# Kernel optimization log

Hardware: AMD Instinct MI355X
Metric: run time of the kernel (lower is better)

Reference implementation:

```python
import jax, jax.numpy as jnp
import numpy as np
from jax import lax

B, S, I, K = 64, 512, 50, 4
H_FC, OUT, H_R = 1024, 128, 512


def setup_inputs() -> dict:
    key = jax.random.key(0)
    ks = jax.random.split(key, 24)
    inp = {}
    inp["x"] = jax.random.normal(ks[0], (B, S, I), dtype=jnp.float32)
    # col 0 = mu, col 1 = sigma (divisor); uniform(0,1) shifted away from 0 for stability
    fp = jax.random.uniform(ks[1], (I * K, 2), dtype=jnp.float32)
    inp["fuzzy_params"] = fp.at[:, 1].add(0.5)
    # FC stack: (I*K -> H_FC), (H_FC -> H_FC) x (num_fc-2=2), (H_FC -> OUT)
    dims = [(H_FC, I * K), (H_FC, H_FC), (H_FC, H_FC), (OUT, H_FC)]
    for j, (o, i) in enumerate(dims):
        inp[f"fc{j}_w"] = jax.random.normal(ks[2 + 2 * j], (o, i), dtype=jnp.float32) * 0.02
        inp[f"fc{j}_b"] = jnp.zeros((o,), dtype=jnp.float32)
    # 2-layer Elman RNN (tanh), batch_first
    inp["w_ih0"] = jax.random.normal(ks[12], (H_R, OUT), dtype=jnp.float32) * 0.04
    inp["w_hh0"] = jax.random.normal(ks[13], (H_R, H_R), dtype=jnp.float32) * 0.04
    inp["b_ih0"] = jnp.zeros((H_R,), dtype=jnp.float32)
    inp["b_hh0"] = jnp.zeros((H_R,), dtype=jnp.float32)
    inp["w_ih1"] = jax.random.normal(ks[14], (H_R, H_R), dtype=jnp.float32) * 0.04
    inp["w_hh1"] = jax.random.normal(ks[15], (H_R, H_R), dtype=jnp.float32) * 0.04
    inp["b_ih1"] = jnp.zeros((H_R,), dtype=jnp.float32)
    inp["b_hh1"] = jnp.zeros((H_R,), dtype=jnp.float32)
    return inp


def _rnn_layer(inp, w_ih, w_hh, b_ih, b_hh):
    # inp: [B,S,D] -> [B,S,H]; precompute input projection, scan recurrence over time
    pre = jnp.einsum("bsd,hd->bsh", inp, w_ih) + b_ih + b_hh

    def step(h, x_t):
        h = jnp.tanh(x_t + h @ w_hh.T)
        return h, h

    h0 = jnp.zeros((inp.shape[0], w_hh.shape[0]), dtype=inp.dtype)
    _, ys = lax.scan(step, h0, jnp.swapaxes(pre, 0, 1))  # [S,B,H]
    return jnp.swapaxes(ys, 0, 1)


def reference(x, fuzzy_params, fc0_w, fc0_b, fc1_w, fc1_b, fc2_w, fc2_b, fc3_w, fc3_b,
              w_ih0, w_hh0, b_ih0, b_hh0, w_ih1, w_hh1, b_ih1, b_hh1):
    # Fuzzy layer: exp(-(x - mu_k)^2 / sigma_k), output ordered as [k, i] flattened
    mu = fuzzy_params[:, 0].reshape(K, I)
    sig = fuzzy_params[:, 1].reshape(K, I)
    z = jnp.exp(-((x[:, :, None, :] - mu) ** 2) / sig)  # [B,S,K,I]
    z = z.reshape(x.shape[0], x.shape[1], K * I)
    # FC stack (no nonlinearity in original)
    for w, b in ((fc0_w, fc0_b), (fc1_w, fc1_b), (fc2_w, fc2_b), (fc3_w, fc3_b)):
        z = z @ w.T + b
    # 2-layer tanh RNN
    z = _rnn_layer(z, w_ih0, w_hh0, b_ih0, b_hh0)
    z = _rnn_layer(z, w_ih1, w_hh1, b_ih1, b_hh1)
    return z
```

## Files before the change

kernel.cpp:

```cpp
#include <hip/hip_runtime.h>
#include <hip/hip_fp16.h>
#include <cstddef>


typedef _Float16 half8 __attribute__((ext_vector_type(8)));
typedef float f32x4 __attribute__((ext_vector_type(4)));
typedef float f32v4 __attribute__((ext_vector_type(4)));
typedef _Float16 v2h __attribute__((ext_vector_type(2)));

__device__ __forceinline__ void gld_lds16(const void* g, void* lds) {
  __builtin_amdgcn_global_load_lds(
      (const __attribute__((address_space(1))) unsigned int*)g,
      (__attribute__((address_space(3))) unsigned int*)lds, 16, 0, 0);
}

__global__ void fuzzy16(const float* __restrict__ x, const float* __restrict__ fp,
                        _Float16* __restrict__ z, int nrows) {
  int idx = blockIdx.x * blockDim.x + threadIdx.x;
  if (idx >= nrows * 256) return;
  int r = idx >> 8;
  int f = idx & 255;
  float v = 0.f;
  if (f < 200) {
    int i = f % 50;
    float xv = x[r * 50 + i];
    float mu = fp[2 * f];
    float sg = fp[2 * f + 1];
    float d = xv - mu;
    v = expf(-(d * d) / sg);
  }
  z[idx] = (_Float16)v;
}

__global__ void cvt_w16(const float* __restrict__ W, _Float16* __restrict__ O,
                        int rows, int kin, int kpad) {
  int idx = blockIdx.x * blockDim.x + threadIdx.x;
  if (idx >= rows * kpad) return;
  int r = idx / kpad;
  int k = idx - r * kpad;
  O[idx] = (k < kin) ? (_Float16)W[(size_t)r * kin + k] : (_Float16)0.f;
}

__global__ __launch_bounds__(256) void gemm16(
    const _Float16* __restrict__ A, const _Float16* __restrict__ W,
    const float* __restrict__ b1, const float* __restrict__ b2,
    _Float16* __restrict__ C, int M, int N, int K) {
  __shared__ _Float16 As[128 * 32];
  __shared__ _Float16 Bs[128 * 32];
  const int tid = threadIdx.x;
  const int bm = blockIdx.y * 128;
  const int bn = blockIdx.x * 128;
  const int lane = tid & 63;
  const int wv = tid >> 6;
  const int wm = (wv >> 1) * 64;
  const int wn = (wv & 1) * 64;
  const int frow = lane & 15;
  const int fk = (lane >> 4) * 8;

  const int srow = tid >> 2;
  const int scol = (tid & 3) * 16;
  const char* gA = (const char*)(A + (size_t)(bm + srow) * K) + scol;
  const char* gB = (const char*)(W + (size_t)(bn + srow) * K) + scol;
  const size_t rowstep = (size_t)64 * K * 2;
  char* lA = (char*)As + tid * 16;
  char* lB = (char*)Bs + tid * 16;

  f32x4 acc[4][4] = {};

  for (int k0 = 0; k0 < K; k0 += 32) {
    gld_lds16(gA, lA);
    gld_lds16(gA + rowstep, lA + 4096);
    gld_lds16(gB, lB);
    gld_lds16(gB + rowstep, lB + 4096);
    gA += 64;
    gB += 64;
    __syncthreads();
    half8 af[4], bf[4];
#pragma unroll
    for (int i = 0; i < 4; i++) {
      af[i] = *(const half8*)(As + (wm + i * 16 + frow) * 32 + fk);
      bf[i] = *(const half8*)(Bs + (wn + i * 16 + frow) * 32 + fk);
    }
#pragma unroll
    for (int i = 0; i < 4; i++)
#pragma unroll
      for (int j = 0; j < 4; j++)
        acc[i][j] = __builtin_amdgcn_mfma_f32_16x16x32_f16(af[i], bf[j], acc[i][j], 0, 0, 0);
    __syncthreads();
  }

  float bias[4];
#pragma unroll
  for (int j = 0; j < 4; j++) {
    int col = bn + wn + j * 16 + frow;
    bias[j] = b1[col] + (b2 ? b2[col] : 0.f);
  }
  const int r0 = (lane >> 4) * 4;
#pragma unroll
  for (int i = 0; i < 4; i++) {
#pragma unroll
    for (int r = 0; r < 4; r++) {
      int row = bm + wm + i * 16 + r0 + r;
      _Float16* Cp = C + (size_t)row * N + bn + wn + frow;
#pragma unroll
      for (int j = 0; j < 4; j++)
        Cp[j * 16] = (_Float16)(acc[i][j][r] + bias[j]);
    }
  }
}

__global__ void pack_whh_fp16(const float* __restrict__ W, float4* __restrict__ QW) {
  int idx = blockIdx.x * blockDim.x + threadIdx.x;
  if (idx >= 32768) return;
  int j4 = idx >> 9;
  int o = idx & 511;
  const float* src = W + (size_t)o * 512 + j4 * 8;
  __align__(16) __half2 p[4];
#pragma unroll
  for (int k = 0; k < 4; k++)
    p[k] = __halves2half2(__float2half(src[2 * k]), __float2half(src[2 * k + 1]));
  QW[idx] = *(const float4*)p;
}

__device__ __forceinline__ float dot2acc(float wbits, float hbits, float acc) {
#if __has_builtin(__builtin_amdgcn_fdot2)
  return __builtin_amdgcn_fdot2(__builtin_bit_cast(v2h, wbits),
                                __builtin_bit_cast(v2h, hbits), acc, false);
#else
  float2 wf = __half22float2(__builtin_bit_cast(__half2, wbits));
  float2 hf = __half22float2(__builtin_bit_cast(__half2, hbits));
  return fmaf(wf.x, hf.x, fmaf(wf.y, hf.y, acc));
#endif
}

#define DECLK(k)                                                           \
  f32x4 w##k##_0 = qb[(0 << 9) + ((k) << 6)]; asm volatile("" : "+v"(w##k##_0)); \
  f32x4 w##k##_1 = qb[(1 << 9) + ((k) << 6)]; asm volatile("" : "+v"(w##k##_1)); \
  f32x4 w##k##_2 = qb[(2 << 9) + ((k) << 6)]; asm volatile("" : "+v"(w##k##_2)); \
  f32x4 w##k##_3 = qb[(3 << 9) + ((k) << 6)]; asm volatile("" : "+v"(w##k##_3)); \
  f32x4 w##k##_4 = qb[(4 << 9) + ((k) << 6)]; asm volatile("" : "+v"(w##k##_4));

#define DOT1(k, g)                                  \
  acc##k = dot2acc(w##k##_##g.x, hq.x, acc##k);     \
  acc##k = dot2acc(w##k##_##g.y, hq.y, acc##k);     \
  acc##k = dot2acc(w##k##_##g.z, hq.z, acc##k);     \
  acc##k = dot2acc(w##k##_##g.w, hq.w, acc##k);

#define DOTG(g)                         \
  {                                     \
    f32v4 hq = hs4[w8 + (g)];           \
    DOT1(0, g) DOT1(1, g) DOT1(2, g)    \
    DOT1(3, g) DOT1(4, g) DOT1(5, g)    \
    DOT1(6, g) DOT1(7, g)               \
  }

#define DOTLK(gp, k)                                \
  {                                                 \
    f32v4 q = wl[((gp) << 9) + ((k) << 6)];         \
    acc##k = dot2acc(q.x, hq.x, acc##k);            \
    acc##k = dot2acc(q.y, hq.y, acc##k);            \
    acc##k = dot2acc(q.z, hq.z, acc##k);            \
    acc##k = dot2acc(q.w, hq.w, acc##k);            \
  }

#define DOTL(gp)                                    \
  {                                                 \
    f32v4 hq = hs4[w8 + 5 + (gp)];                  \
    DOTLK(gp, 0) DOTLK(gp, 1) DOTLK(gp, 2)          \
    DOTLK(gp, 3) DOTLK(gp, 4) DOTLK(gp, 5)          \
    DOTLK(gp, 6) DOTLK(gp, 7)                       \
  }

#define DOTS(k)                                     \
  acc##k = dot2acc(s##k.x, hq.x, acc##k);           \
  acc##k = dot2acc(s##k.y, hq.y, acc##k);           \
  acc##k = dot2acc(s##k.z, hq.z, acc##k);           \
  acc##k = dot2acc(s##k.w, hq.w, acc##k);

__global__ __attribute__((amdgpu_flat_work_group_size(512, 512),
                          amdgpu_waves_per_eu(2, 2)))
void rnn_r9_k(
    const _Float16* __restrict__ pre,
    const f32v4* __restrict__ QW,
    float* __restrict__ out32,
    _Float16* __restrict__ out16) {
  const int b = blockIdx.x;
  const int tid = threadIdx.x;
  const int w = tid >> 6;
  const int l = tid & 63;
  const int w8 = w << 3;

  __shared__ f32v4 wlds[16][512];
  __shared__ float psum[8][512];
  __shared__ __align__(16) __half hbuf[2][512];

  const f32v4* qb = QW + ((size_t)(w8) << 9) + l;
  DECLK(0) DECLK(1) DECLK(2) DECLK(3) DECLK(4) DECLK(5) DECLK(6) DECLK(7)

  f32v4* wl = &wlds[w << 1][l];
#pragma unroll
  for (int gp = 0; gp < 2; gp++)
#pragma unroll
    for (int k = 0; k < 8; k++)
      wl[(gp << 9) + (k << 6)] = qb[((5 + gp) << 9) + (k << 6)];

  const f32v4* q7 = qb + (7 << 9);

  hbuf[0][tid] = __float2half(0.f);
  __syncthreads();

  const _Float16* preb = pre + (size_t)b * 262144;
  float* ob32 = out32 ? out32 + (size_t)b * 262144 : nullptr;
  _Float16* ob16 = out16 ? out16 + (size_t)b * 262144 : nullptr;

  _Float16 pcur = preb[tid];
  int p = 0;
  for (int t = 0; t < 512; t++) {
    const f32v4* hs4 = (const f32v4*)hbuf[p];
    f32x4 s0 = q7[0 << 6], s1 = q7[1 << 6], s2 = q7[2 << 6], s3 = q7[3 << 6];
    f32x4 s4 = q7[4 << 6], s5 = q7[5 << 6], s6 = q7[6 << 6], s7 = q7[7 << 6];
    float acc0 = 0.f, acc1 = 0.f, acc2 = 0.f, acc3 = 0.f;
    float acc4 = 0.f, acc5 = 0.f, acc6 = 0.f, acc7 = 0.f;
    DOTG(0) DOTG(1) DOTG(2) DOTG(3) DOTG(4)
    DOTL(0) DOTL(1)
    {
      f32v4 hq = hs4[w8 + 7];
      DOTS(0) DOTS(1) DOTS(2) DOTS(3) DOTS(4) DOTS(5) DOTS(6) DOTS(7)
    }
    float* ps = &psum[w][l];
    ps[0] = acc0;   ps[64] = acc1;  ps[128] = acc2; ps[192] = acc3;
    ps[256] = acc4; ps[320] = acc5; ps[384] = acc6; ps[448] = acc7;
    __syncthreads();
    float s = (float)pcur;
    if (t < 511) pcur = preb[(t + 1) * 512 + tid];
    s += psum[0][tid] + psum[1][tid] + psum[2][tid] + psum[3][tid] +
         psum[4][tid] + psum[5][tid] + psum[6][tid] + psum[7][tid];
    float z = __expf(2.f * s);
    float r = __builtin_amdgcn_rcpf(z + 1.f);
    float hn = fmaf(-2.f, r, 1.f);
    hbuf[p ^ 1][tid] = __float2half(hn);
    if (ob32) ob32[t * 512 + tid] = hn;
    if (ob16) ob16[t * 512 + tid] = (_Float16)hn;
    p ^= 1;
    __syncthreads();
  }
}

extern "C" void kernel_launch(void* const* d_in, const int* in_sizes, int n_in,
                              void* d_out, int out_size, void* d_ws, size_t ws_size,
                              hipStream_t stream) {
  const float* x     = (const float*)d_in[0];
  const float* fp    = (const float*)d_in[1];
  const float* fc0_w = (const float*)d_in[2];
  const float* fc0_b = (const float*)d_in[3];
  const float* fc1_w = (const float*)d_in[4];
  const float* fc1_b = (const float*)d_in[5];
  const float* fc2_w = (const float*)d_in[6];
  const float* fc2_b = (const float*)d_in[7];
  const float* fc3_w = (const float*)d_in[8];
  const float* fc3_b = (const float*)d_in[9];
  const float* w_ih0 = (const float*)d_in[10];
  const float* w_hh0 = (const float*)d_in[11];
  const float* b_ih0 = (const float*)d_in[12];
  const float* b_hh0 = (const float*)d_in[13];
  const float* w_ih1 = (const float*)d_in[14];
  const float* w_hh1 = (const float*)d_in[15];
  const float* b_ih1 = (const float*)d_in[16];
  const float* b_hh1 = (const float*)d_in[17];
  float* out = (float*)d_out;
  float* ws  = (float*)d_ws;

  _Float16* preH = (_Float16*)ws;
  float* U = ws + 8388608;
  _Float16* h16 = (_Float16*)U;
  _Float16* t0  = (_Float16*)U;
  float* R2 = U + 4194304;
  _Float16* t1  = (_Float16*)R2;
  _Float16* zc  = (_Float16*)R2;
  _Float16* f3  = (_Float16*)(R2 + 1048576);
  float* wbase = ws + 16777216;
  float4*   QW0   = (float4*)wbase;
  float4*   QW1   = (float4*)(wbase + 131072);
  _Float16* fc0h  = (_Float16*)(wbase + 262144);
  _Float16* fc1h  = (_Float16*)(wbase + 393216);
  _Float16* fc2h  = (_Float16*)(wbase + 917504);
  _Float16* fc3h  = (_Float16*)(wbase + 1441792);
  _Float16* wih0h = (_Float16*)(wbase + 1507328);
  _Float16* wih1h = (_Float16*)(wbase + 1540096);

  pack_whh_fp16<<<128, 256, 0, stream>>>(w_hh0, QW0);
  pack_whh_fp16<<<128, 256, 0, stream>>>(w_hh1, QW1);
  cvt_w16<<<1024, 256, 0, stream>>>(fc0_w, fc0h, 1024, 200, 256);
  cvt_w16<<<4096, 256, 0, stream>>>(fc1_w, fc1h, 1024, 1024, 1024);
  cvt_w16<<<4096, 256, 0, stream>>>(fc2_w, fc2h, 1024, 1024, 1024);
  cvt_w16<<<512, 256, 0, stream>>>(fc3_w, fc3h, 128, 1024, 1024);
  cvt_w16<<<256, 256, 0, stream>>>(w_ih0, wih0h, 512, 128, 128);
  cvt_w16<<<1024, 256, 0, stream>>>(w_ih1, wih1h, 512, 512, 512);

  const int CH = 8192;
  for (int c = 0; c < 4; c++) {
    size_t row0 = (size_t)c * CH;
    fuzzy16<<<CH, 256, 0, stream>>>(x + row0 * 50, fp, zc, CH);
    gemm16<<<dim3(8, 64), 256, 0, stream>>>(zc, fc0h, fc0_b, nullptr, t0, CH, 1024, 256);
    gemm16<<<dim3(8, 64), 256, 0, stream>>>(t0, fc1h, fc1_b, nullptr, t1, CH, 1024, 1024);
    gemm16<<<dim3(8, 64), 256, 0, stream>>>(t1, fc2h, fc2_b, nullptr, t0, CH, 1024, 1024);
    gemm16<<<dim3(1, 64), 256, 0, stream>>>(t0, fc3h, fc3_b, nullptr, f3, CH, 128, 1024);
    gemm16<<<dim3(4, 64), 256, 0, stream>>>(f3, wih0h, b_ih0, b_hh0,
                                            preH + row0 * 512, CH, 512, 128);
  }

  rnn_r9_k<<<64, 512, 0, stream>>>(preH, (const f32v4*)QW0, nullptr, h16);
  gemm16<<<dim3(4, 256), 256, 0, stream>>>(h16, wih1h, b_ih1, b_hh1, preH, 32768, 512, 512);
  rnn_r9_k<<<64, 512, 0, stream>>>(preH, (const f32v4*)QW1, out, nullptr);
}
```

Before: 2.126 ms.

## Pipeline both RNN layers and the layer-1 input projection in one persistent kernel

Replaces the sequence of RNN layer 0, the w_ih1 GEMM and RNN layer 1 with a single 192-block kernel. The blocks form three stages per batch row: the layer-0 recurrence, a per-timestep w_ih1 projection, and the layer-1 recurrence. Stages pass data through global inboxes and a ring buffer, synchronised with flag counters and spin-waits. This lets the two sequential recurrences overlap in time instead of running back to back. It relies on all 192 blocks being co-resident, since a non-resident block would deadlock the spin-waits, and it adds spin polling and per-step matvec work for the projection stage.

```diff
diff --git a/kernel.cpp b/kernel.cpp
--- a/kernel.cpp
+++ b/kernel.cpp
@@ -133,6 +133,15 @@
 #endif
 }
 
+__device__ __forceinline__ unsigned int spin_until(unsigned int* f, unsigned int need) {
+  unsigned int v = __hip_atomic_load(f, __ATOMIC_RELAXED, __HIP_MEMORY_SCOPE_AGENT);
+  while (v < need) {
+    __builtin_amdgcn_s_sleep(8);
+    v = __hip_atomic_load(f, __ATOMIC_RELAXED, __HIP_MEMORY_SCOPE_AGENT);
+  }
+  return v;
+}
+
 #define DECLK(k)                                                           \
   f32x4 w##k##_0 = qb[(0 << 9) + ((k) << 6)]; asm volatile("" : "+v"(w##k##_0)); \
   f32x4 w##k##_1 = qb[(1 << 9) + ((k) << 6)]; asm volatile("" : "+v"(w##k##_1)); \
@@ -177,14 +186,23 @@
   acc##k = dot2acc(s##k.z, hq.z, acc##k);           \
   acc##k = dot2acc(s##k.w, hq.w, acc##k);
 
+#define RING_MASK 63
+
 __global__ __attribute__((amdgpu_flat_work_group_size(512, 512),
                           amdgpu_waves_per_eu(2, 2)))
-void rnn_r9_k(
-    const _Float16* __restrict__ pre,
-    const f32v4* __restrict__ QW,
+void rnn_pipe3_k(
+    const _Float16* __restrict__ pre0,
+    const f32v4* __restrict__ QWA,
+    const f32v4* __restrict__ QWB,
+    const f32v4* __restrict__ QWC,
+    const float* __restrict__ bih1, const float* __restrict__ bhh1,
+    _Float16* __restrict__ inbox0,
+    _Float16* __restrict__ inbox1,
     float* __restrict__ out32,
-    _Float16* __restrict__ out16) {
-  const int b = blockIdx.x;
+    unsigned int* __restrict__ flags) {
+  const int bid = blockIdx.x;
+  const int stage = bid >> 6;
+  const int b = bid & 63;
   const int tid = threadIdx.x;
   const int w = tid >> 6;
   const int l = tid & 63;
@@ -194,6 +212,7 @@
   __shared__ float psum[8][512];
   __shared__ __align__(16) __half hbuf[2][512];
 
+  const f32v4* QW = (stage == 0) ? QWA : (stage == 1) ? QWB : QWC;
   const f32v4* qb = QW + ((size_t)(w8) << 9) + l;
   DECLK(0) DECLK(1) DECLK(2) DECLK(3) DECLK(4) DECLK(5) DECLK(6) DECLK(7)
 
@@ -203,20 +222,59 @@
 #pragma unroll
     for (int k = 0; k < 8; k++)
       wl[(gp << 9) + (k << 6)] = qb[((5 + gp) << 9) + (k << 6)];
-
   const f32v4* q7 = qb + (7 << 9);
 
-  hbuf[0][tid] = __float2half(0.f);
+  unsigned int* inflag  = (stage == 1) ? (flags + b) : (flags + 64 + b);
+  unsigned int* outflag = (stage == 0) ? (flags + b) : (flags + 64 + b);
+  unsigned long long* in0b = (unsigned long long*)(inbox0 + ((size_t)b << 18));
+  unsigned int* out0b = (unsigned int*)(inbox0 + ((size_t)b << 18));
+  unsigned int* io1b = (unsigned int*)(inbox1 + ((size_t)b << 15));
+  const _Float16* preb = pre0 + ((size_t)b << 18);
+  float* ob32 = out32 + ((size_t)b << 18);
+
+  unsigned int fw = 0;
+  float bias = 0.f;
+  _Float16 pcur = (_Float16)0.f;
+  unsigned long long xv = 0;
+
+  if (stage == 0) {
+    pcur = preb[tid];
+    hbuf[0][tid] = __float2half(0.f);
+  } else if (stage == 1) {
+    bias = bih1[tid] + bhh1[tid];
+    fw = spin_until(inflag, 1u);
+    asm volatile("" ::: "memory");
+    if (tid < 128) {
+      unsigned long long v = __hip_atomic_load(in0b + tid, __ATOMIC_RELAXED,
+                                               __HIP_MEMORY_SCOPE_AGENT);
+      ((unsigned long long*)hbuf[0])[tid] = v;
+    }
+  } else {
+    hbuf[0][tid] = __float2half(0.f);
+    fw = spin_until(inflag, 1u);
+    asm volatile("" ::: "memory");
+    unsigned int pv = __hip_atomic_load(io1b + (tid >> 1), __ATOMIC_RELAXED,
+                                        __HIP_MEMORY_SCOPE_AGENT);
+    unsigned short us = (tid & 1) ? (unsigned short)(pv >> 16)
+                                  : (unsigned short)(pv & 0xffffu);
+    pcur = __builtin_bit_cast(_Float16, us);
+  }
   __syncthreads();
 
-  const _Float16* preb = pre + (size_t)b * 262144;
-  float* ob32 = out32 ? out32 + (size_t)b * 262144 : nullptr;
-  _Float16* ob16 = out16 ? out16 + (size_t)b * 262144 : nullptr;
-
-  _Float16 pcur = preb[tid];
   int p = 0;
   for (int t = 0; t < 512; t++) {
     const f32v4* hs4 = (const f32v4*)hbuf[p];
+    unsigned int fwnew = fw;
+    if (stage != 0)
+      fwnew = __hip_atomic_load(inflag, __ATOMIC_RELAXED, __HIP_MEMORY_SCOPE_AGENT);
+    int xv_ok = 0;
+    if (stage == 1 && t < 511 && fw >= (unsigned)(t + 2)) {
+      asm volatile("" ::: "memory");
+      if (tid < 128)
+        xv = __hip_atomic_load(in0b + (((size_t)(t + 1)) << 7) + tid,
+                               __ATOMIC_RELAXED, __HIP_MEMORY_SCOPE_AGENT);
+      xv_ok = 1;
+    }
     f32x4 s0 = q7[0 << 6], s1 = q7[1 << 6], s2 = q7[2 << 6], s3 = q7[3 << 6];
     f32x4 s4 = q7[4 << 6], s5 = q7[5 << 6], s6 = q7[6 << 6], s7 = q7[7 << 6];
     float acc0 = 0.f, acc1 = 0.f, acc2 = 0.f, acc3 = 0.f;
@@ -231,18 +289,70 @@
     ps[0] = acc0;   ps[64] = acc1;  ps[128] = acc2; ps[192] = acc3;
     ps[256] = acc4; ps[320] = acc5; ps[384] = acc6; ps[448] = acc7;
     __syncthreads();
-    float s = (float)pcur;
-    if (t < 511) pcur = preb[(t + 1) * 512 + tid];
-    s += psum[0][tid] + psum[1][tid] + psum[2][tid] + psum[3][tid] +
-         psum[4][tid] + psum[5][tid] + psum[6][tid] + psum[7][tid];
-    float z = __expf(2.f * s);
-    float r = __builtin_amdgcn_rcpf(z + 1.f);
-    float hn = fmaf(-2.f, r, 1.f);
-    hbuf[p ^ 1][tid] = __float2half(hn);
-    if (ob32) ob32[t * 512 + tid] = hn;
-    if (ob16) ob16[t * 512 + tid] = (_Float16)hn;
+    float sum = psum[0][tid] + psum[1][tid] + psum[2][tid] + psum[3][tid] +
+                psum[4][tid] + psum[5][tid] + psum[6][tid] + psum[7][tid];
+
+    if (stage == 0) {
+      float s = (float)pcur + sum;
+      if (t < 511) pcur = preb[(t + 1) * 512 + tid];
+      float z = __expf(2.f * s);
+      float hn = fmaf(-2.f, __builtin_amdgcn_rcpf(z + 1.f), 1.f);
+      float hn2 = __shfl_down(hn, 1);
+      if (!(tid & 1)) {
+        __half2 pr = __halves2half2(__float2half(hn), __float2half(hn2));
+        __hip_atomic_store(out0b + (((size_t)t) << 8) + (tid >> 1),
+                           __builtin_bit_cast(unsigned int, pr),
+                           __ATOMIC_RELAXED, __HIP_MEMORY_SCOPE_AGENT);
+      }
+      hbuf[p ^ 1][tid] = __float2half(hn);
+    } else if (stage == 1) {
+      float s = bias + sum;
+      float s2 = __shfl_down(s, 1);
+      if (!(tid & 1)) {
+        __half2 pr = __halves2half2(__float2half(s), __float2half(s2));
+        __hip_atomic_store(io1b + (((size_t)(t & RING_MASK)) << 8) + (tid >> 1),
+                           __builtin_bit_cast(unsigned int, pr),
+                           __ATOMIC_RELAXED, __HIP_MEMORY_SCOPE_AGENT);
+      }
+      if (t < 511) {
+        if (!xv_ok) {
+          unsigned int need = (unsigned)(t + 2);
+          unsigned int fx = (fwnew > fw) ? fwnew : fw;
+          if (fx < need) fx = spin_until(inflag, need);
+          fw = fx;
+          asm volatile("" ::: "memory");
+          if (tid < 128)
+            xv = __hip_atomic_load(in0b + (((size_t)(t + 1)) << 7) + tid,
+                                   __ATOMIC_RELAXED, __HIP_MEMORY_SCOPE_AGENT);
+        }
+        if (tid < 128) ((unsigned long long*)hbuf[p ^ 1])[tid] = xv;
+      }
+    } else {
+      float s = (float)pcur + sum;
+      float z = __expf(2.f * s);
+      float hn = fmaf(-2.f, __builtin_amdgcn_rcpf(z + 1.f), 1.f);
+      ob32[t * 512 + tid] = hn;
+      hbuf[p ^ 1][tid] = __float2half(hn);
+      if (t < 511) {
+        unsigned int need = (unsigned)(t + 2);
+        unsigned int fx = (fwnew > fw) ? fwnew : fw;
+        if (fx < need) fx = spin_until(inflag, need);
+        fw = fx;
+        asm volatile("" ::: "memory");
+        unsigned int pv = __hip_atomic_load(
+            io1b + (((size_t)((t + 1) & RING_MASK)) << 8) + (tid >> 1),
+            __ATOMIC_RELAXED, __HIP_MEMORY_SCOPE_AGENT);
+        unsigned short us = (tid & 1) ? (unsigned short)(pv >> 16)
+                                      : (unsigned short)(pv & 0xffffu);
+        pcur = __builtin_bit_cast(_Float16, us);
+      }
+    }
+    if (stage != 0) fw = (fwnew > fw) ? fwnew : fw;
     p ^= 1;
     __syncthreads();
+    if (stage != 2 && tid == 0)
+      __hip_atomic_store(outflag, (unsigned)(t + 1), __ATOMIC_RELEASE,
+                         __HIP_MEMORY_SCOPE_AGENT);
   }
 }
 
@@ -286,16 +396,18 @@
   _Float16* fc2h  = (_Float16*)(wbase + 917504);
   _Float16* fc3h  = (_Float16*)(wbase + 1441792);
   _Float16* wih0h = (_Float16*)(wbase + 1507328);
-  _Float16* wih1h = (_Float16*)(wbase + 1540096);
+  float4*   QWB   = (float4*)(wbase + 1540096);
+  _Float16* inbox1 = (_Float16*)(wbase + 393216);
+  unsigned int* flagsBase = (unsigned int*)fc0h;
 
   pack_whh_fp16<<<128, 256, 0, stream>>>(w_hh0, QW0);
   pack_whh_fp16<<<128, 256, 0, stream>>>(w_hh1, QW1);
+  pack_whh_fp16<<<128, 256, 0, stream>>>(w_ih1, QWB);
   cvt_w16<<<1024, 256, 0, stream>>>(fc0_w, fc0h, 1024, 200, 256);
   cvt_w16<<<4096, 256, 0, stream>>>(fc1_w, fc1h, 1024, 1024, 1024);
   cvt_w16<<<4096, 256, 0, stream>>>(fc2_w, fc2h, 1024, 1024, 1024);
   cvt_w16<<<512, 256, 0, stream>>>(fc3_w, fc3h, 128, 1024, 1024);
   cvt_w16<<<256, 256, 0, stream>>>(w_ih0, wih0h, 512, 128, 128);
-  cvt_w16<<<1024, 256, 0, stream>>>(w_ih1, wih1h, 512, 512, 512);
 
   const int CH = 8192;
   for (int c = 0; c < 4; c++) {
@@ -309,7 +421,8 @@
                                             preH + row0 * 512, CH, 512, 128);
   }
 
-  rnn_r9_k<<<64, 512, 0, stream>>>(preH, (const f32v4*)QW0, nullptr, h16);
-  gemm16<<<dim3(4, 256), 256, 0, stream>>>(h16, wih1h, b_ih1, b_hh1, preH, 32768, 512, 512);
-  rnn_r9_k<<<64, 512, 0, stream>>>(preH, (const f32v4*)QW1, out, nullptr);
-}
+  hipMemsetAsync((void*)flagsBase, 0, 128 * sizeof(unsigned int), stream);
+  rnn_pipe3_k<<<192, 512, 0, stream>>>(
+      preH, (const f32v4*)QW0, (const f32v4*)QWB, (const f32v4*)QW1,
+      b_ih1, b_hh1, h16, inbox1, out, flagsBase);
+}
```

After: 3.571 ms. 68.0% more time.
